# Optimization experiments

Measured on AMD Instinct MI355X. Metric: run time of the kernel, lower is better.

Reference implementation:

```python
import jax, jax.numpy as jnp
import numpy as np

DIM = 320; HEADS = 8; DHEAD = 40; CTX_DIM = 768
INNER = HEADS * DHEAD; FF_INNER = 4 * DIM
B = 1; N = 4096; M = 77
SCALE = DHEAD ** -0.5


def setup_inputs() -> dict:
    key = jax.random.key(0)
    ks = jax.random.split(key, 16)
    p = lambda i, shape: jax.random.normal(ks[i], shape, dtype=jnp.float32) * 0.02
    return {
        "x": jax.random.normal(ks[0], (B, N, DIM), dtype=jnp.float32),
        "context": jax.random.normal(ks[1], (B, M, CTX_DIM), dtype=jnp.float32),
        "focused_attention_mask": jax.random.uniform(ks[2], (1, M, M), dtype=jnp.float32),
        "g1": jnp.ones((DIM,), jnp.float32), "b1": jnp.zeros((DIM,), jnp.float32),
        "g2": jnp.ones((DIM,), jnp.float32), "b2": jnp.zeros((DIM,), jnp.float32),
        "g3": jnp.ones((DIM,), jnp.float32), "b3": jnp.zeros((DIM,), jnp.float32),
        "Wq1": p(3, (DIM, INNER)), "Wk1": p(4, (DIM, INNER)), "Wv1": p(5, (DIM, INNER)),
        "Wo1": p(6, (INNER, DIM)), "bo1": jnp.zeros((DIM,), jnp.float32),
        "Wq2": p(7, (DIM, INNER)), "Wk2": p(8, (CTX_DIM, INNER)), "Wv2": p(9, (CTX_DIM, INNER)),
        "Wo2": p(10, (INNER, DIM)), "bo2": jnp.zeros((DIM,), jnp.float32),
        "Wff1": p(11, (DIM, 2 * FF_INNER)), "bff1": jnp.zeros((2 * FF_INNER,), jnp.float32),
        "Wff2": p(12, (FF_INNER, DIM)), "bff2": jnp.zeros((DIM,), jnp.float32),
        "use_fca": 1,
    }


def _ln(x, g, b):
    mu = x.mean(-1, keepdims=True)
    var = jnp.mean((x - mu) ** 2, -1, keepdims=True)
    return (x - mu) * jax.lax.rsqrt(var + 1e-5) * g + b


def _attn(xn, ctx, Wq, Wk, Wv, Wo, bo, fam, use_fca):
    b, n, _ = xn.shape
    heads = lambda t: t.reshape(b, t.shape[1], HEADS, DHEAD).transpose(0, 2, 1, 3)  # b h n d
    q, k, v = heads(xn @ Wq), heads(ctx @ Wk), heads(ctx @ Wv)
    sim = jnp.einsum('bhid,bhjd->bhij', q, k) * SCALE
    if use_fca:
        m = fam.shape[-1]  # fam: [1, m, m], batch must be 1 (repeat_interleave semantics)
        fw = jnp.einsum('bhqk,dk->bhqd', sim[..., :m], fam[0])
        fw = jnp.minimum(jnp.abs(fw), 1.0)
        fw = fw / (jnp.max(fw, axis=-1, keepdims=True) + 1e-6)
        fw = (fw > 0.6).astype(sim.dtype)
        sim = sim.at[..., :m].add((fw - 1.0) * 50.0)
    a = jax.nn.softmax(sim, axis=-1)
    o = jnp.einsum('bhij,bhjd->bhid', a, v).transpose(0, 2, 1, 3).reshape(b, n, INNER)
    return o @ Wo + bo


def reference(x, context, focused_attention_mask,
              g1, b1, g2, b2, g3, b3,
              Wq1, Wk1, Wv1, Wo1, bo1,
              Wq2, Wk2, Wv2, Wo2, bo2,
              Wff1, bff1, Wff2, bff2, use_fca):
    # attn1: self-attention (context=None in original -> use_fca forced to 0)
    h1 = _ln(x, g1, b1)
    x = _attn(h1, h1, Wq1, Wk1, Wv1, Wo1, bo1, None, 0) + x
    # attn2: cross-attention with focused-attention mask
    h2 = _ln(x, g2, b2)
    x = _attn(h2, context, Wq2, Wk2, Wv2, Wo2, bo2, focused_attention_mask, int(use_fca)) + x
    # GEGLU feed-forward
    h3 = _ln(x, g3, b3)
    proj = h3 @ Wff1 + bff1
    a_, gate = jnp.split(proj, 2, axis=-1)
    x = (a_ * jax.nn.gelu(gate, approximate=False)) @ Wff2 + bff2 + x
    return x
```

## Files before the change

### kernel.cpp

```cpp
#include <hip/hip_runtime.h>
#include <math.h>

typedef __bf16 bf16_t;
typedef __bf16 bf16x8 __attribute__((ext_vector_type(8)));
typedef __bf16 bf16x4 __attribute__((ext_vector_type(4)));
typedef float  f32x4  __attribute__((ext_vector_type(4)));
typedef _Float16 f16_t;
typedef _Float16 f16x4 __attribute__((ext_vector_type(4)));
typedef _Float16 f16x8 __attribute__((ext_vector_type(8)));
typedef __fp16 hf16x2 __attribute__((ext_vector_type(2)));

static constexpr float ATT_SCALE = 0.15811388300841897f;
static constexpr float SC2 = 0.22811031f;
static constexpr float LOG2E = 1.4426950408889634f;

__device__ __forceinline__ bf16_t f2b(float f) {
  unsigned u = __float_as_uint(f);
  u = (u + 0x7fffu + ((u >> 16) & 1u)) >> 16;
  unsigned short s = (unsigned short)u;
  bf16_t r;
  *(unsigned short*)&r = s;
  return r;
}
__device__ __forceinline__ float b2f(bf16_t b) {
  unsigned short s = *(const unsigned short*)&b;
  return __uint_as_float(((unsigned)s) << 16);
}
__device__ __forceinline__ void sto(float v, float* p)  { *p = v; }
__device__ __forceinline__ void sto(float v, bf16_t* p) { *p = f2b(v); }
__device__ __forceinline__ unsigned pkh2(float a, float b) {
  hf16x2 h = __builtin_amdgcn_cvt_pkrtz(a, b);
  return *(unsigned*)&h;
}

__global__ __launch_bounds__(256) void prep_kernel(
    const float* __restrict__ Wq1, const float* __restrict__ Wk1, const float* __restrict__ Wv1,
    const float* __restrict__ Wo1, const float* __restrict__ Wq2,
    const float* __restrict__ Wk2, const float* __restrict__ Wv2, const float* __restrict__ Wo2,
    const float* __restrict__ Wff1, const float* __restrict__ Wff2,
    const float* __restrict__ fam,
    bf16_t* __restrict__ wqkvt, bf16_t* __restrict__ wo1t, float* __restrict__ wkv2t,
    bf16_t* __restrict__ wo2t, bf16_t* __restrict__ wff1t, bf16_t* __restrict__ wff2t,
    bf16_t* __restrict__ wq2th, bf16_t* __restrict__ wq2tl,
    bf16_t* __restrict__ famh, bf16_t* __restrict__ faml,
    bf16_t* __restrict__ zpad)
{
  const int T1 = 960*320;
  const int T2 = T1 + 320*320;
  const int T3 = T2 + 768*640;
  const int T4 = T3 + 320*320;
  const int T5 = T4 + 2560*320;
  const int T6 = T5 + 320*1280;
  const int T7 = T6 + 320*320;
  const int T8 = T7 + 96*96;
  const int T9 = T8 + 135168;
  for (int i = blockIdx.x*256 + threadIdx.x; i < T9; i += gridDim.x*256) {
    if (i < T1) {
      int n = i / 320, k = i - n*320;
      float v = (n < 320) ? Wq1[k*320+n] * SC2
              : (n < 640) ? Wk1[k*320+n-320] : Wv1[k*320+n-640];
      wqkvt[i] = f2b(v);
    } else if (i < T2) {
      int e = i - T1; int n = e / 320, k = e - n*320;
      wo1t[e] = f2b(Wo1[k*320+n]);
    } else if (i < T3) {
      int e = i - T2; int n = e / 768, k = e - n*768;
      wkv2t[e] = (n < 320) ? Wk2[k*320+n] : Wv2[k*320+n-320];
    } else if (i < T4) {
      int e = i - T3; int n = e / 320, k = e - n*320;
      wo2t[e] = f2b(Wo2[k*320+n]);
    } else if (i < T5) {
      int e = i - T4; int n = e / 320, k = e - n*320;
      wff1t[e] = f2b(Wff1[(size_t)k*2560+n]);
    } else if (i < T6) {
      int e = i - T5; int n = e / 1280, k = e - n*1280;
      wff2t[e] = f2b(Wff2[k*320+n]);
    } else if (i < T7) {
      int e = i - T6; int n = e / 320, k = e - n*320;
      float v = Wq2[k*320+n];
      bf16_t h = f2b(v);
      wq2th[e] = h;
      wq2tl[e] = f2b(v - b2f(h));
    } else if (i < T8) {
      int e = i - T7; int d = e / 96, k = e - d*96;
      float v = (d < 77 && k < 77) ? fam[d*77 + k] : 0.f;
      bf16_t h = f2b(v);
      famh[e] = h;
      faml[e] = f2b(v - b2f(h));
    } else {
      zpad[i - T8] = f2b(0.f);
    }
  }
}

template<typename OT>
__global__ __launch_bounds__(256) void ln_kernel(
    const float* __restrict__ x, const float* __restrict__ g, const float* __restrict__ b,
    OT* __restrict__ out)
{
  const int lane = threadIdx.x & 63;
  const int row = blockIdx.x * 4 + (threadIdx.x >> 6);
  const float* xr = x + (size_t)row * 320;
  float v[5], s = 0.f, s2 = 0.f;
#pragma unroll
  for (int i = 0; i < 5; i++) { v[i] = xr[lane + i*64]; s += v[i]; s2 += v[i]*v[i]; }
#pragma unroll
  for (int o = 32; o; o >>= 1) { s += __shfl_xor(s, o); s2 += __shfl_xor(s2, o); }
  float mu = s * (1.f/320.f);
  float rs = rsqrtf(fmaxf(s2*(1.f/320.f) - mu*mu, 0.f) + 1e-5f);
#pragma unroll
  for (int i = 0; i < 5; i++) {
    int c = lane + i*64;
    sto((v[i]-mu)*rs*g[c] + b[c], &out[(size_t)row*320 + c]);
  }
}

__global__ __launch_bounds__(256) void ln2_split_kernel(
    const float* __restrict__ x, const float* __restrict__ g, const float* __restrict__ b,
    bf16_t* __restrict__ hi, bf16_t* __restrict__ lo)
{
  const int lane = threadIdx.x & 63;
  const int row = blockIdx.x * 4 + (threadIdx.x >> 6);
  const float* xr = x + (size_t)row * 320;
  float v[5], s = 0.f, s2 = 0.f;
#pragma unroll
  for (int i = 0; i < 5; i++) { v[i] = xr[lane + i*64]; s += v[i]; s2 += v[i]*v[i]; }
#pragma unroll
  for (int o = 32; o; o >>= 1) { s += __shfl_xor(s, o); s2 += __shfl_xor(s2, o); }
  float mu = s * (1.f/320.f);
  float rs = rsqrtf(fmaxf(s2*(1.f/320.f) - mu*mu, 0.f) + 1e-5f);
#pragma unroll
  for (int i = 0; i < 5; i++) {
    int c = lane + i*64;
    float y = (v[i]-mu)*rs*g[c] + b[c];
    bf16_t h = f2b(y);
    hi[(size_t)row*320 + c] = h;
    lo[(size_t)row*320 + c] = f2b(y - b2f(h));
  }
}

__global__ __launch_bounds__(256) void kv2_dot_kernel(
    const float* __restrict__ ctx, const float* __restrict__ wkv2t,
    bf16_t* __restrict__ k2h, bf16_t* __restrict__ k2l, bf16_t* __restrict__ v2t)
{
  const int gid = blockIdx.x*16 + (threadIdx.x >> 4);
  const int q = threadIdx.x & 15;
  const int m = gid / 640, n = gid - m*640;
  const float4* a = (const float4*)(ctx + (size_t)m*768);
  const float4* b = (const float4*)(wkv2t + (size_t)n*768);
  float acc = 0.f;
#pragma unroll
  for (int i = 0; i < 12; i++) {
    float4 av = a[i*16+q], bv = b[i*16+q];
    acc += av.x*bv.x + av.y*bv.y + av.z*bv.z + av.w*bv.w;
  }
#pragma unroll
  for (int o = 8; o; o >>= 1) acc += __shfl_xor(acc, o);
  if (q == 0) {
    if (n < 320) {
      int h = n / 40, d = n - h*40;
      int i = h*6144 + m*64 + d;
      bf16_t hh = f2b(acc);
      k2h[i] = hh;
      k2l[i] = f2b(acc - b2f(hh));
    } else {
      int n2 = n - 320; int h = n2 / 40, d = n2 - h*40;
      v2t[h*4608 + d*96 + m] = f2b(acc);
    }
  }
}

__global__ __launch_bounds__(256) void repack_vt_kernel(
    const bf16_t* __restrict__ qkvb, f16_t* __restrict__ vpack, bf16_t* __restrict__ kpack)
{
  __shared__ f16_t T[64*44];
  const int tid = threadIdx.x;
  const int t0 = blockIdx.x * 64, h = blockIdx.y;
  for (int e = tid; e < 320; e += 256) {
    int t = e / 5, c8 = (e - t*5) * 8;
    bf16x8 v = *(const bf16x8*)(qkvb + (size_t)(t0+t)*960 + 640 + h*40 + c8);
    f16_t* dst = &T[t*44 + c8];
#pragma unroll
    for (int j = 0; j < 8; j++) dst[j] = (f16_t)b2f(v[j]);
  }
  __syncthreads();
  for (int e = tid; e < 3072; e += 256) {
    int dt = e >> 10;
    int r  = e & 1023;
    int g2 = r >> 9, o = r & 511;
    int lane = o >> 3, j = o & 7;
    int qd = lane >> 4, ln = lane & 15;
    int d = dt*16 + ln;
    int key = g2*32 + ((j & 4) ? 16 : 0) + qd*4 + (j & 3);
    float val;
    if (d < 40)       val = (float)T[key*44 + d];
    else if (d == 40) val = 1.0f;
    else              val = 0.0f;
    vpack[(((size_t)h*3 + dt)*128 + (t0 >> 5) + g2)*512 + o] = (f16_t)val;
  }
  for (int e = tid; e < 2560; e += 256) {
    int g = e / 640, o = e - g*640;
    int key = t0 + g*16;
    bf16_t val;
    if (o < 512) {
      int lane = o >> 3, j = o & 7;
      int qd = lane >> 4, ln = lane & 15;
      val = qkvb[(size_t)(key + ln)*960 + 320 + h*40 + qd*8 + j];
    } else {
      int o2 = o - 512; int ln = o2 >> 3, j = o2 & 7;
      val = qkvb[(size_t)(key + ln)*960 + 320 + h*40 + 32 + j];
    }
    kpack[((size_t)h*256 + (t0 >> 4) + g)*640 + o] = val;
  }
}

__global__ __launch_bounds__(256, 4) void flash_self_kernel(
    const bf16_t* __restrict__ qkvb, const bf16_t* __restrict__ kpack,
    const f16_t* __restrict__ vpack,
    float* __restrict__ opart, float* __restrict__ lpart)
{
  __shared__ float Red[6144];
  const int tid = threadIdx.x;
  const int w = tid >> 6, lane = tid & 63;
  const int ln = lane & 15, qd = lane >> 4;
  const int qh = w >> 1, kh = w & 1;
  const int h = blockIdx.x & 7;
  const int q0 = (blockIdx.x >> 3) * 64;
  const int split = blockIdx.y;

  const int kgbase = h*256 + kh*2;
  const int vgbase = h*384 + kh;
  const int lko = lane*8;

  bf16x8 zero8 = {};
  bf16x8 bq[2][2];
#pragma unroll
  for (int nt = 0; nt < 2; nt++) {
    const bf16_t* qp = qkvb + (size_t)(q0 + qh*32 + nt*16 + ln)*960 + h*40;
    bq[nt][0] = *(const bf16x8*)(qp + qd*8);
    bq[nt][1] = (qd == 0) ? *(const bf16x8*)(qp + 32) : zero8;
  }

  f32x4 zero4 = {0.f,0.f,0.f,0.f};
  f32x4 oacc[3][2];
#pragma unroll
  for (int a = 0; a < 3; a++)
#pragma unroll
    for (int b = 0; b < 2; b++) oacc[a][b] = zero4;

#define FS_LOADK(DST, K0)                                                       \
  {                                                                             \
    const bf16_t* kp_ = kpack + ((size_t)kgbase + ((K0) >> 4)) * 640;           \
    DST[0][0] = *(const bf16x8*)(kp_ + lko);                                    \
    DST[0][1] = (qd == 0) ? *(const bf16x8*)(kp_ + 512 + ln*8) : zero8;         \
    DST[1][0] = *(const bf16x8*)(kp_ + 640 + lko);                              \
    DST[1][1] = (qd == 0) ? *(const bf16x8*)(kp_ + 1152 + ln*8) : zero8;        \
  }

#define FS_LOADV(DST, K0)                                                       \
  {                                                                             \
    _Pragma("unroll")                                                           \
    for (int dt_ = 0; dt_ < 3; dt_++)                                           \
      DST[dt_] = *(const f16x8*)(vpack + ((size_t)vgbase + dt_*128 + ((K0) >> 5)) * 512 + lko); \
  }

#define FS_COMPUTE(KA, VA)                                                      \
  {                                                                             \
    _Pragma("unroll")                                                           \
    for (int nt = 0; nt < 2; nt++) {                                            \
      f32x4 s0 = __builtin_amdgcn_mfma_f32_16x16x32_bf16(KA[0][0], bq[nt][0], zero4, 0,0,0); \
      s0 = __builtin_amdgcn_mfma_f32_16x16x32_bf16(KA[0][1], bq[nt][1], s0, 0,0,0); \
      f32x4 s1 = __builtin_amdgcn_mfma_f32_16x16x32_bf16(KA[1][0], bq[nt][0], zero4, 0,0,0); \
      s1 = __builtin_amdgcn_mfma_f32_16x16x32_bf16(KA[1][1], bq[nt][1], s1, 0,0,0); \
      uint4 u_;                                                                 \
      u_.x = pkh2(__builtin_amdgcn_exp2f(s0[0]), __builtin_amdgcn_exp2f(s0[1])); \
      u_.y = pkh2(__builtin_amdgcn_exp2f(s0[2]), __builtin_amdgcn_exp2f(s0[3])); \
      u_.z = pkh2(__builtin_amdgcn_exp2f(s1[0]), __builtin_amdgcn_exp2f(s1[1])); \
      u_.w = pkh2(__builtin_amdgcn_exp2f(s1[2]), __builtin_amdgcn_exp2f(s1[3])); \
      f16x8 pb = *(f16x8*)&u_;                                                  \
      _Pragma("unroll")                                                         \
      for (int dt = 0; dt < 3; dt++)                                            \
        oacc[dt][nt] = __builtin_amdgcn_mfma_f32_16x16x32_f16(VA[dt], pb, oacc[dt][nt], 0,0,0); \
    }                                                                           \
  }

  bf16x8 ka[2][2], kb[2][2];
  f16x8 va[3], vb[3];
  FS_LOADK(ka, split*2048);
#pragma unroll 1
  for (int kt = 0; kt < 32; kt += 2) {
    const int k0 = split*2048 + kt*64;
    FS_LOADV(va, k0);
    FS_LOADK(kb, k0 + 64);
    FS_COMPUTE(ka, va);
    FS_LOADV(vb, k0 + 64);
    FS_LOADK(ka, (kt + 2 < 32) ? (k0 + 128) : split*2048);
    FS_COMPUTE(kb, vb);
  }
#undef FS_LOADK
#undef FS_LOADV
#undef FS_COMPUTE

#pragma unroll
  for (int nt = 0; nt < 2; nt++)
#pragma unroll
    for (int dt = 0; dt < 3; dt++)
      *(f32x4*)&Red[((w*2 + nt)*3 + dt)*256 + ln*16 + qd*4] = oacc[dt][nt];
  __syncthreads();
  float* obase = opart + ((size_t)(split*8 + h)*4096 + q0)*40;
  const int qh2 = tid >> 7, lq = (tid >> 3) & 15, dbase = tid & 7;
#pragma unroll
  for (int nt = 0; nt < 2; nt++) {
#pragma unroll
    for (int i = 0; i < 5; i++) {
      int d = dbase + i*8;
      int dt = d >> 4, dr = d & 15;
      float v = Red[(((qh2*2 + 0)*2 + nt)*3 + dt)*256 + lq*16 + dr]
              + Red[(((qh2*2 + 1)*2 + nt)*3 + dt)*256 + lq*16 + dr];
      obase[(size_t)(qh2*32 + nt*16 + lq)*40 + d] = v;
    }
    if (dbase == 0) {
      float l = Red[(((qh2*2 + 0)*2 + nt)*3 + 2)*256 + lq*16 + 8]
              + Red[(((qh2*2 + 1)*2 + nt)*3 + 2)*256 + lq*16 + 8];
      lpart[(size_t)(split*8 + h)*4096 + q0 + qh2*32 + nt*16 + lq] = l;
    }
  }
}

__global__ __launch_bounds__(256) void merge_o1_kernel(
    const float* __restrict__ op, const float* __restrict__ lp, bf16_t* __restrict__ o1a)
{
  int i = blockIdx.x*256 + threadIdx.x;
  int q = i / 320, c = i - q*320;
  int h = c / 40, d = c - h*40;
  size_t base = ((size_t)h*4096 + q)*40 + d;
  float l = lp[h*4096 + q] + lp[32768 + h*4096 + q];
  float o = op[base] + op[base + 1310720];
  o1a[i] = f2b(o / l);
}

__global__ __launch_bounds__(256) void attn_cross_kernel(
    const float* __restrict__ q2, const bf16_t* __restrict__ k2h, const bf16_t* __restrict__ k2l,
    const bf16_t* __restrict__ famh, const bf16_t* __restrict__ faml,
    const bf16_t* __restrict__ v2t, const int* __restrict__ use_fca,
    bf16_t* __restrict__ o2)
{
  __shared__ bf16_t SMh[4][16*96];
  __shared__ bf16_t SMl[4][16*96];
  __shared__ bf16_t PAs[4][16*96];
  const int tid = threadIdx.x;
  const int w = tid >> 6, lane = tid & 63;
  const int ln = lane & 15, qd = lane >> 4;
  const int h = blockIdx.x & 7;
  const int q0 = (blockIdx.x >> 3)*64 + w*16;
  const int fca = use_fca[0];
  bf16_t* smh = SMh[w];
  bf16_t* sml = SMl[w];
  bf16_t* pa  = PAs[w];

  {
    bf16x4 z = {};
    int q = lane >> 2, c = 80 + (lane & 3)*4;
    *(bf16x4*)&smh[q*96 + c] = z;
    *(bf16x4*)&sml[q*96 + c] = z;
    *(bf16x4*)&pa [q*96 + c] = z;
  }

  bf16x8 zero8 = {};
  bf16x8 aqh0, aql0, aqh1 = zero8, aql1 = zero8;
  {
    const float* qp = q2 + (size_t)(q0 + ln)*320 + h*40;
    float4 v0 = *(const float4*)(qp + qd*8);
    float4 v1 = *(const float4*)(qp + qd*8 + 4);
    float qv[8] = {v0.x,v0.y,v0.z,v0.w,v1.x,v1.y,v1.z,v1.w};
#pragma unroll
    for (int i = 0; i < 8; i++) {
      bf16_t hh = f2b(qv[i]);
      aqh0[i] = hh; aql0[i] = f2b(qv[i] - b2f(hh));
    }
    if (qd == 0) {
      float4 u0 = *(const float4*)(qp + 32);
      float4 u1 = *(const float4*)(qp + 36);
      float uv[8] = {u0.x,u0.y,u0.z,u0.w,u1.x,u1.y,u1.z,u1.w};
#pragma unroll
      for (int i = 0; i < 8; i++) {
        bf16_t hh = f2b(uv[i]);
        aqh1[i] = hh; aql1[i] = f2b(uv[i] - b2f(hh));
      }
    }
  }

  f32x4 zero4 = {0.f,0.f,0.f,0.f};
  float ss[5][4];
#pragma unroll
  for (int nt = 0; nt < 5; nt++) {
    const bf16_t* kb = k2h + ((size_t)h*96 + nt*16 + ln)*64 + qd*8;
    const bf16_t* kl = k2l + ((size_t)h*96 + nt*16 + ln)*64 + qd*8;
    bf16x8 kh0 = *(const bf16x8*)kb;
    bf16x8 kh1 = *(const bf16x8*)(kb + 32);
    bf16x8 kl0 = *(const bf16x8*)kl;
    bf16x8 kl1 = *(const bf16x8*)(kl + 32);
    f32x4 s;
    s = __builtin_amdgcn_mfma_f32_16x16x32_bf16(aqh0, kl0, zero4, 0, 0, 0);
    s = __builtin_amdgcn_mfma_f32_16x16x32_bf16(aql0, kh0, s, 0, 0, 0);
    s = __builtin_amdgcn_mfma_f32_16x16x32_bf16(aqh0, kh0, s, 0, 0, 0);
    s = __builtin_amdgcn_mfma_f32_16x16x32_bf16(aqh1, kl1, s, 0, 0, 0);
    s = __builtin_amdgcn_mfma_f32_16x16x32_bf16(aql1, kh1, s, 0, 0, 0);
    s = __builtin_amdgcn_mfma_f32_16x16x32_bf16(aqh1, kh1, s, 0, 0, 0);
#pragma unroll
    for (int r = 0; r < 4; r++) {
      float sv = s[r] * ATT_SCALE;
      ss[nt][r] = sv;
      bf16_t hh = f2b(sv);
      smh[(qd*4 + r)*96 + nt*16 + ln] = hh;
      sml[(qd*4 + r)*96 + nt*16 + ln] = f2b(sv - b2f(hh));
    }
  }

  f32x4 facc[5];
#pragma unroll
  for (int nt = 0; nt < 5; nt++) facc[nt] = zero4;
#pragma unroll
  for (int c = 0; c < 3; c++) {
    bf16x8 sah = *(const bf16x8*)&smh[ln*96 + c*32 + qd*8];
    bf16x8 sal = *(const bf16x8*)&sml[ln*96 + c*32 + qd*8];
#pragma unroll
    for (int nt = 0; nt < 5; nt++) {
      bf16x8 fh8 = *(const bf16x8*)(famh + ((size_t)(nt*16 + ln))*96 + c*32 + qd*8);
      bf16x8 fl8 = *(const bf16x8*)(faml + ((size_t)(nt*16 + ln))*96 + c*32 + qd*8);
      facc[nt] = __builtin_amdgcn_mfma_f32_16x16x32_bf16(sah, fl8, facc[nt], 0, 0, 0);
      facc[nt] = __builtin_amdgcn_mfma_f32_16x16x32_bf16(sal, fh8, facc[nt], 0, 0, 0);
      facc[nt] = __builtin_amdgcn_mfma_f32_16x16x32_bf16(sah, fh8, facc[nt], 0, 0, 0);
    }
  }

  float pr[5][4];
  if (fca) {
    float fwv[5][4], fm[4];
#pragma unroll
    for (int nt = 0; nt < 5; nt++)
#pragma unroll
      for (int r = 0; r < 4; r++) fwv[nt][r] = fminf(fabsf(facc[nt][r]), 1.f);
#pragma unroll
    for (int r = 0; r < 4; r++) {
      float m = fmaxf(fmaxf(fwv[0][r], fwv[1][r]), fmaxf(fwv[2][r], fmaxf(fwv[3][r], fwv[4][r])));
#pragma unroll
      for (int o = 8; o; o >>= 1) m = fmaxf(m, __shfl_xor(m, o));
      fm[r] = m;
    }
#pragma unroll
    for (int nt = 0; nt < 5; nt++)
#pragma unroll
      for (int r = 0; r < 4; r++) {
        float lg = ss[nt][r] - ((fwv[nt][r] > 0.6f*(fm[r] + 1e-6f)) ? 0.f : 50.f);
        pr[nt][r] = __builtin_amdgcn_exp2f(lg * LOG2E);
      }
  } else {
#pragma unroll
    for (int nt = 0; nt < 5; nt++)
#pragma unroll
      for (int r = 0; r < 4; r++)
        pr[nt][r] = __builtin_amdgcn_exp2f(ss[nt][r] * LOG2E);
  }
  if (ln >= 13) {
#pragma unroll
    for (int r = 0; r < 4; r++) pr[4][r] = 0.f;
  }
  float l_[4] = {0.f,0.f,0.f,0.f};
#pragma unroll
  for (int nt = 0; nt < 5; nt++)
#pragma unroll
    for (int r = 0; r < 4; r++) {
      l_[r] += pr[nt][r];
      pa[(qd*4 + r)*96 + nt*16 + ln] = f2b(pr[nt][r]);
    }
#pragma unroll
  for (int r = 0; r < 4; r++)
#pragma unroll
    for (int o = 8; o; o >>= 1) l_[r] += __shfl_xor(l_[r], o);

  f32x4 oacc[3];
#pragma unroll
  for (int nt = 0; nt < 3; nt++) oacc[nt] = zero4;
#pragma unroll
  for (int c = 0; c < 3; c++) {
    bf16x8 paf = *(const bf16x8*)&pa[ln*96 + c*32 + qd*8];
#pragma unroll
    for (int nt = 0; nt < 3; nt++) {
      bf16x8 vb = *(const bf16x8*)(v2t + ((size_t)h*48 + nt*16 + ln)*96 + c*32 + qd*8);
      oacc[nt] = __builtin_amdgcn_mfma_f32_16x16x32_bf16(paf, vb, oacc[nt], 0, 0, 0);
    }
  }
  float inv[4];
#pragma unroll
  for (int r = 0; r < 4; r++) inv[r] = 1.f / l_[r];
#pragma unroll
  for (int nt = 0; nt < 3; nt++) {
    int d = nt*16 + ln;
    if (d < 40) {
#pragma unroll
      for (int r = 0; r < 4; r++)
        o2[(size_t)(q0 + qd*4 + r)*320 + h*40 + d] = f2b(oacc[nt][r]*inv[r]);
    }
  }
}

template<int OUT_BF16>
__global__ __launch_bounds__(256) void gemm_bf16_kernel(
    const bf16_t* __restrict__ A, const bf16_t* __restrict__ Bt,
    const float* __restrict__ bias, const float* __restrict__ resid,
    void* __restrict__ Cout, int M, int N, int K)
{
  __shared__ bf16_t As[128][72];
  __shared__ bf16_t Bs[64][72];
  const int tid = threadIdx.x;
  const int m0 = blockIdx.x * 128, n0 = blockIdx.y * 64;
  const int w = tid >> 6, lane = tid & 63;
  const int wr = w >> 1, wc = w & 1;
  const int ln = lane & 15, qd = lane >> 4;
  f32x4 zero = {0.f, 0.f, 0.f, 0.f};
  f32x4 acc[4][2];
#pragma unroll
  for (int a = 0; a < 4; a++)
#pragma unroll
    for (int b = 0; b < 2; b++) acc[a][b] = zero;

  for (int k0 = 0; k0 < K; k0 += 64) {
    __syncthreads();
#pragma unroll
    for (int i = 0; i < 4; i++) {
      int vid = tid + i*256;
      int r = vid >> 3, c8 = (vid & 7) * 8;
      *(bf16x8*)&As[r][c8] = *(const bf16x8*)(A + (size_t)(m0+r)*K + k0 + c8);
    }
#pragma unroll
    for (int i = 0; i < 2; i++) {
      int vid = tid + i*256;
      int r = vid >> 3, c8 = (vid & 7) * 8;
      *(bf16x8*)&Bs[r][c8] = *(const bf16x8*)(Bt + (size_t)(n0+r)*K + k0 + c8);
    }
    __syncthreads();
#pragma unroll
    for (int c = 0; c < 2; c++) {
      bf16x8 af[4], bfr[2];
#pragma unroll
      for (int mt = 0; mt < 4; mt++)
        af[mt] = *(const bf16x8*)&As[wr*64 + mt*16 + ln][c*32 + qd*8];
#pragma unroll
      for (int nt = 0; nt < 2; nt++)
        bfr[nt] = *(const bf16x8*)&Bs[wc*32 + nt*16 + ln][c*32 + qd*8];
#pragma unroll
      for (int mt = 0; mt < 4; mt++)
#pragma unroll
        for (int nt = 0; nt < 2; nt++)
          acc[mt][nt] = __builtin_amdgcn_mfma_f32_16x16x32_bf16(af[mt], bfr[nt], acc[mt][nt], 0, 0, 0);
    }
  }
#pragma unroll
  for (int mt = 0; mt < 4; mt++)
#pragma unroll
    for (int nt = 0; nt < 2; nt++)
#pragma unroll
      for (int r = 0; r < 4; r++) {
        int gm = m0 + wr*64 + mt*16 + qd*4 + r;
        int gn = n0 + wc*32 + nt*16 + ln;
        float v = acc[mt][nt][r];
        if (bias)  v += bias[gn];
        if (resid) v += resid[(size_t)gm*N + gn];
        if (OUT_BF16) sto(v, &((bf16_t*)Cout)[(size_t)gm*N + gn]);
        else          sto(v, &((float*)Cout)[(size_t)gm*N + gn]);
      }
}

template<int OUT_BF16>
__global__ __launch_bounds__(256) void gemm_bf16_32_kernel(
    const bf16_t* __restrict__ A, const bf16_t* __restrict__ Bt,
    const float* __restrict__ bias, const float* __restrict__ resid,
    void* __restrict__ Cout, int M, int N, int K)
{
  __shared__ bf16_t As[32][72];
  __shared__ bf16_t Bs[64][72];
  const int tid = threadIdx.x;
  const int m0 = blockIdx.x * 32, n0 = blockIdx.y * 64;
  const int w = tid >> 6, lane = tid & 63;
  const int wr = w >> 1, wc = w & 1;
  const int ln = lane & 15, qd = lane >> 4;
  f32x4 zero = {0.f, 0.f, 0.f, 0.f};
  f32x4 acc[2];
  acc[0] = zero; acc[1] = zero;

  for (int k0 = 0; k0 < K; k0 += 64) {
    __syncthreads();
    {
      int r = tid >> 3, c8 = (tid & 7) * 8;
      *(bf16x8*)&As[r][c8] = *(const bf16x8*)(A + (size_t)(m0+r)*K + k0 + c8);
    }
#pragma unroll
    for (int i = 0; i < 2; i++) {
      int vid = tid + i*256;
      int r = vid >> 3, c8 = (vid & 7) * 8;
      *(bf16x8*)&Bs[r][c8] = *(const bf16x8*)(Bt + (size_t)(n0+r)*K + k0 + c8);
    }
    __syncthreads();
#pragma unroll
    for (int c = 0; c < 2; c++) {
      bf16x8 af = *(const bf16x8*)&As[wr*16 + ln][c*32 + qd*8];
#pragma unroll
      for (int nt = 0; nt < 2; nt++) {
        bf16x8 bfr = *(const bf16x8*)&Bs[wc*32 + nt*16 + ln][c*32 + qd*8];
        acc[nt] = __builtin_amdgcn_mfma_f32_16x16x32_bf16(af, bfr, acc[nt], 0, 0, 0);
      }
    }
  }
#pragma unroll
  for (int nt = 0; nt < 2; nt++)
#pragma unroll
    for (int r = 0; r < 4; r++) {
      int gm = m0 + wr*16 + qd*4 + r;
      int gn = n0 + wc*32 + nt*16 + ln;
      float v = acc[nt][r];
      if (bias)  v += bias[gn];
      if (resid) v += resid[(size_t)gm*N + gn];
      if (OUT_BF16) sto(v, &((bf16_t*)Cout)[(size_t)gm*N + gn]);
      else          sto(v, &((float*)Cout)[(size_t)gm*N + gn]);
    }
}

__global__ __launch_bounds__(256) void gemm3_32_kernel(
    const bf16_t* __restrict__ Ah, const bf16_t* __restrict__ Al,
    const bf16_t* __restrict__ Bth, const bf16_t* __restrict__ Btl,
    float* __restrict__ C, int M, int N, int K)
{
  __shared__ bf16_t Ash[32][72];
  __shared__ bf16_t Asl[32][72];
  __shared__ bf16_t Bsh[64][72];
  __shared__ bf16_t Bsl[64][72];
  const int tid = threadIdx.x;
  const int m0 = blockIdx.x * 32, n0 = blockIdx.y * 64;
  const int w = tid >> 6, lane = tid & 63;
  const int wr = w >> 1, wc = w & 1;
  const int ln = lane & 15, qd = lane >> 4;
  f32x4 zero = {0.f, 0.f, 0.f, 0.f};
  f32x4 acc[2];
  acc[0] = zero; acc[1] = zero;

  for (int k0 = 0; k0 < K; k0 += 64) {
    __syncthreads();
    {
      int r = tid >> 3, c8 = (tid & 7) * 8;
      *(bf16x8*)&Ash[r][c8] = *(const bf16x8*)(Ah + (size_t)(m0+r)*K + k0 + c8);
      *(bf16x8*)&Asl[r][c8] = *(const bf16x8*)(Al + (size_t)(m0+r)*K + k0 + c8);
    }
#pragma unroll
    for (int i = 0; i < 2; i++) {
      int vid = tid + i*256;
      int r = vid >> 3, c8 = (vid & 7) * 8;
      *(bf16x8*)&Bsh[r][c8] = *(const bf16x8*)(Bth + (size_t)(n0+r)*K + k0 + c8);
      *(bf16x8*)&Bsl[r][c8] = *(const bf16x8*)(Btl + (size_t)(n0+r)*K + k0 + c8);
    }
    __syncthreads();
#pragma unroll
    for (int c = 0; c < 2; c++) {
      bf16x8 afh = *(const bf16x8*)&Ash[wr*16 + ln][c*32 + qd*8];
      bf16x8 afl = *(const bf16x8*)&Asl[wr*16 + ln][c*32 + qd*8];
#pragma unroll
      for (int nt = 0; nt < 2; nt++) {
        bf16x8 bfh = *(const bf16x8*)&Bsh[wc*32 + nt*16 + ln][c*32 + qd*8];
        bf16x8 bfl = *(const bf16x8*)&Bsl[wc*32 + nt*16 + ln][c*32 + qd*8];
        acc[nt] = __builtin_amdgcn_mfma_f32_16x16x32_bf16(afh, bfl, acc[nt], 0, 0, 0);
        acc[nt] = __builtin_amdgcn_mfma_f32_16x16x32_bf16(afl, bfh, acc[nt], 0, 0, 0);
        acc[nt] = __builtin_amdgcn_mfma_f32_16x16x32_bf16(afh, bfh, acc[nt], 0, 0, 0);
      }
    }
  }
#pragma unroll
  for (int nt = 0; nt < 2; nt++)
#pragma unroll
    for (int r = 0; r < 4; r++) {
      int gm = m0 + wr*16 + qd*4 + r;
      int gn = n0 + wc*32 + nt*16 + ln;
      C[(size_t)gm*N + gn] = acc[nt][r];
    }
}

__global__ __launch_bounds__(256) void gemm_geglu_kernel(
    const bf16_t* __restrict__ A, const bf16_t* __restrict__ Bt,
    const float* __restrict__ bias, bf16_t* __restrict__ gg, int K)
{
  __shared__ bf16_t As[128][72];
  __shared__ bf16_t Ba[64][72];
  __shared__ bf16_t Bg[64][72];
  const int tid = threadIdx.x;
  const int m0 = blockIdx.x * 128, n0 = blockIdx.y * 64;
  const int w = tid >> 6, lane = tid & 63;
  const int wr = w >> 1, wc = w & 1;
  const int ln = lane & 15, qd = lane >> 4;
  f32x4 zero = {0.f, 0.f, 0.f, 0.f};
  f32x4 acca[4][2], accg[4][2];
#pragma unroll
  for (int a = 0; a < 4; a++)
#pragma unroll
    for (int b = 0; b < 2; b++) { acca[a][b] = zero; accg[a][b] = zero; }

  for (int k0 = 0; k0 < K; k0 += 64) {
    __syncthreads();
#pragma unroll
    for (int i = 0; i < 4; i++) {
      int vid = tid + i*256;
      int r = vid >> 3, c8 = (vid & 7) * 8;
      *(bf16x8*)&As[r][c8] = *(const bf16x8*)(A + (size_t)(m0+r)*K + k0 + c8);
    }
#pragma unroll
    for (int i = 0; i < 2; i++) {
      int vid = tid + i*256;
      int r = vid >> 3, c8 = (vid & 7) * 8;
      *(bf16x8*)&Ba[r][c8] = *(const bf16x8*)(Bt + (size_t)(n0+r)*K + k0 + c8);
      *(bf16x8*)&Bg[r][c8] = *(const bf16x8*)(Bt + (size_t)(n0+r+1280)*K + k0 + c8);
    }
    __syncthreads();
#pragma unroll
    for (int c = 0; c < 2; c++) {
      bf16x8 af[4], ba[2], bg[2];
#pragma unroll
      for (int mt = 0; mt < 4; mt++)
        af[mt] = *(const bf16x8*)&As[wr*64 + mt*16 + ln][c*32 + qd*8];
#pragma unroll
      for (int nt = 0; nt < 2; nt++) {
        ba[nt] = *(const bf16x8*)&Ba[wc*32 + nt*16 + ln][c*32 + qd*8];
        bg[nt] = *(const bf16x8*)&Bg[wc*32 + nt*16 + ln][c*32 + qd*8];
      }
#pragma unroll
      for (int mt = 0; mt < 4; mt++)
#pragma unroll
        for (int nt = 0; nt < 2; nt++) {
          acca[mt][nt] = __builtin_amdgcn_mfma_f32_16x16x32_bf16(af[mt], ba[nt], acca[mt][nt], 0, 0, 0);
          accg[mt][nt] = __builtin_amdgcn_mfma_f32_16x16x32_bf16(af[mt], bg[nt], accg[mt][nt], 0, 0, 0);
        }
    }
  }
#pragma unroll
  for (int mt = 0; mt < 4; mt++)
#pragma unroll
    for (int nt = 0; nt < 2; nt++)
#pragma unroll
      for (int r = 0; r < 4; r++) {
        int gm = m0 + wr*64 + mt*16 + qd*4 + r;
        int gn = n0 + wc*32 + nt*16 + ln;
        float va = acca[mt][nt][r] + bias[gn];
        float vg = accg[mt][nt][r] + bias[1280 + gn];
        float ge = 0.5f * vg * (1.f + erff(vg * 0.70710678118654752f));
        gg[(size_t)gm*1280 + gn] = f2b(va * ge);
      }
}

extern "C" void kernel_launch(void* const* d_in, const int* in_sizes, int n_in,
                              void* d_out, int out_size, void* d_ws, size_t ws_size,
                              hipStream_t stream)
{
  const float* x    = (const float*)d_in[0];
  const float* ctx  = (const float*)d_in[1];
  const float* fam  = (const float*)d_in[2];
  const float* g1   = (const float*)d_in[3];
  const float* b1   = (const float*)d_in[4];
  const float* g2   = (const float*)d_in[5];
  const float* b2   = (const float*)d_in[6];
  const float* g3   = (const float*)d_in[7];
  const float* b3   = (const float*)d_in[8];
  const float* Wq1  = (const float*)d_in[9];
  const float* Wk1  = (const float*)d_in[10];
  const float* Wv1  = (const float*)d_in[11];
  const float* Wo1  = (const float*)d_in[12];
  const float* bo1  = (const float*)d_in[13];
  const float* Wq2  = (const float*)d_in[14];
  const float* Wk2  = (const float*)d_in[15];
  const float* Wv2  = (const float*)d_in[16];
  const float* Wo2  = (const float*)d_in[17];
  const float* bo2  = (const float*)d_in[18];
  const float* Wff1 = (const float*)d_in[19];
  const float* bff1 = (const float*)d_in[20];
  const float* Wff2 = (const float*)d_in[21];
  const float* bff2 = (const float*)d_in[22];
  const int*   ufca = (const int*)d_in[23];

  char* ws = (char*)d_ws;
  bf16_t* qkvb = (bf16_t*)(ws + 0);
  f16_t*  vpack = (f16_t*)(ws + 7864320);
  bf16_t* o1a  = (bf16_t*)(ws + 11010048);
  bf16_t* kpack = (bf16_t*)(ws + 11010048);
  bf16_t* h1b  = (bf16_t*)(ws + 13631488);
  bf16_t* h2hi = (bf16_t*)(ws + 16252928);
  bf16_t* h2lo = (bf16_t*)(ws + 18874368);
  float*  x2   = (float*)(ws + 21495808);
  float*  q2   = (float*)(ws + 26738688);
  bf16_t* o2   = (bf16_t*)(ws + 32178688);
  float*  x3   = (float*)(ws + 34800128);
  bf16_t* h3b  = (bf16_t*)(ws + 40043008);
  bf16_t* wqkvt = (bf16_t*)(ws + 42664448);
  bf16_t* wo1t  = (bf16_t*)(ws + 43278848);
  float*  wkv2t = (float*)(ws + 43483648);
  bf16_t* wo2t  = (bf16_t*)(ws + 45449728);
  bf16_t* wff1t = (bf16_t*)(ws + 45654528);
  bf16_t* wff2t = (bf16_t*)(ws + 47292928);
  float*  lpart = (float*)(ws + 48112128);
  bf16_t* wq2th = (bf16_t*)(ws + 48374272);
  bf16_t* wq2tl = (bf16_t*)(ws + 48579072);
  bf16_t* famh  = (bf16_t*)(ws + 48783872);
  bf16_t* faml  = (bf16_t*)(ws + 48802304);
  bf16_t* k2h   = (bf16_t*)(ws + 48820736);
  bf16_t* k2l   = (bf16_t*)(ws + 48919040);
  bf16_t* v2t   = (bf16_t*)(ws + 49017344);
  float*  opart = (float*)(ws + 21495808);
  bf16_t* gg   = (bf16_t*)(ws + 21495808);

  float* xout = (float*)d_out;

  prep_kernel<<<2048, 256, 0, stream>>>(Wq1, Wk1, Wv1, Wo1, Wq2, Wk2, Wv2, Wo2, Wff1, Wff2, fam,
                                        wqkvt, wo1t, wkv2t, wo2t, wff1t, wff2t, wq2th, wq2tl,
                                        famh, faml, k2h);
  ln_kernel<bf16_t><<<1024, 256, 0, stream>>>(x, g1, b1, h1b);
  gemm_bf16_kernel<1><<<dim3(32,15), 256, 0, stream>>>(h1b, wqkvt, nullptr, nullptr, qkvb, 4096, 960, 320);
  repack_vt_kernel<<<dim3(64,8), 256, 0, stream>>>(qkvb, vpack, kpack);
  flash_self_kernel<<<dim3(512,2), 256, 0, stream>>>(qkvb, kpack, vpack, opart, lpart);
  merge_o1_kernel<<<5120, 256, 0, stream>>>(opart, lpart, o1a);
  gemm_bf16_32_kernel<0><<<dim3(128,5), 256, 0, stream>>>(o1a, wo1t, bo1, x, x2, 4096, 320, 320);
  ln2_split_kernel<<<1024, 256, 0, stream>>>(x2, g2, b2, h2hi, h2lo);
  gemm3_32_kernel<<<dim3(128,5), 256, 0, stream>>>(h2hi, h2lo, wq2th, wq2tl, q2, 4096, 320, 320);
  kv2_dot_kernel<<<3080, 256, 0, stream>>>(ctx, wkv2t, k2h, k2l, v2t);
  attn_cross_kernel<<<512, 256, 0, stream>>>(q2, k2h, k2l, famh, faml, v2t, ufca, o2);
  gemm_bf16_32_kernel<0><<<dim3(128,5), 256, 0, stream>>>(o2, wo2t, bo2, x2, x3, 4096, 320, 320);
  ln_kernel<bf16_t><<<1024, 256, 0, stream>>>(x3, g3, b3, h3b);
  gemm_geglu_kernel<<<dim3(32,20), 256, 0, stream>>>(h3b, wff1t, bff1, gg, 320);
  gemm_bf16_32_kernel<0><<<dim3(128,5), 256, 0, stream>>>(gg, wff2t, bff2, x3, xout, 4096, 320, 1280);
}
```

Baseline: 274.6 us.

## Replace grid-level split-K in self-attention with in-block 4-way key split and fused merge

The self-attention kernel previously split the key range across two grid blocks, wrote fp32 partial outputs and row sums to global memory, and then ran a separate merge kernel. Now each block uses 512 threads (8 waves), with 4 waves per query half covering interleaved key chunks across the full key range. The partials are reduced in shared memory and normalized, and bf16 output is written directly. This removes a kernel launch and the fp32 partial round trip, in exchange for larger blocks, twice the shared memory, and half as many blocks in the grid.

```diff
diff --git a/kernel.cpp b/kernel.cpp
--- a/kernel.cpp
+++ b/kernel.cpp
@@ -214,19 +214,18 @@
   }
 }
 
-__global__ __launch_bounds__(256, 4) void flash_self_kernel(
+__global__ __launch_bounds__(512, 4) void flash_self_kernel(
     const bf16_t* __restrict__ qkvb, const bf16_t* __restrict__ kpack,
     const f16_t* __restrict__ vpack,
-    float* __restrict__ opart, float* __restrict__ lpart)
-{
-  __shared__ float Red[6144];
+    bf16_t* __restrict__ o1a)
+{
+  __shared__ float Red[12288];
   const int tid = threadIdx.x;
   const int w = tid >> 6, lane = tid & 63;
   const int ln = lane & 15, qd = lane >> 4;
-  const int qh = w >> 1, kh = w & 1;
+  const int qh = w >> 2, kh = w & 3;
   const int h = blockIdx.x & 7;
   const int q0 = (blockIdx.x >> 3) * 64;
-  const int split = blockIdx.y;
 
   const int kgbase = h*256 + kh*2;
   const int vgbase = h*384 + kh;
@@ -286,15 +285,15 @@
 
   bf16x8 ka[2][2], kb[2][2];
   f16x8 va[3], vb[3];
-  FS_LOADK(ka, split*2048);
+  FS_LOADK(ka, 0);
 #pragma unroll 1
-  for (int kt = 0; kt < 32; kt += 2) {
-    const int k0 = split*2048 + kt*64;
+  for (int it = 0; it < 32; it += 2) {
+    const int k0 = it*128;
     FS_LOADV(va, k0);
-    FS_LOADK(kb, k0 + 64);
+    FS_LOADK(kb, k0 + 128);
     FS_COMPUTE(ka, va);
-    FS_LOADV(vb, k0 + 64);
-    FS_LOADK(ka, (kt + 2 < 32) ? (k0 + 128) : split*2048);
+    FS_LOADV(vb, k0 + 128);
+    FS_LOADK(ka, (it + 2 < 32) ? (k0 + 256) : 0);
     FS_COMPUTE(kb, vb);
   }
 #undef FS_LOADK
@@ -307,36 +306,23 @@
     for (int dt = 0; dt < 3; dt++)
       *(f32x4*)&Red[((w*2 + nt)*3 + dt)*256 + ln*16 + qd*4] = oacc[dt][nt];
   __syncthreads();
-  float* obase = opart + ((size_t)(split*8 + h)*4096 + q0)*40;
-  const int qh2 = tid >> 7, lq = (tid >> 3) & 15, dbase = tid & 7;
-#pragma unroll
-  for (int nt = 0; nt < 2; nt++) {
-#pragma unroll
-    for (int i = 0; i < 5; i++) {
-      int d = dbase + i*8;
-      int dt = d >> 4, dr = d & 15;
-      float v = Red[(((qh2*2 + 0)*2 + nt)*3 + dt)*256 + lq*16 + dr]
-              + Red[(((qh2*2 + 1)*2 + nt)*3 + dt)*256 + lq*16 + dr];
-      obase[(size_t)(qh2*32 + nt*16 + lq)*40 + d] = v;
-    }
-    if (dbase == 0) {
-      float l = Red[(((qh2*2 + 0)*2 + nt)*3 + 2)*256 + lq*16 + 8]
-              + Red[(((qh2*2 + 1)*2 + nt)*3 + 2)*256 + lq*16 + 8];
-      lpart[(size_t)(split*8 + h)*4096 + q0 + qh2*32 + nt*16 + lq] = l;
-    }
-  }
-}
-
-__global__ __launch_bounds__(256) void merge_o1_kernel(
-    const float* __restrict__ op, const float* __restrict__ lp, bf16_t* __restrict__ o1a)
-{
-  int i = blockIdx.x*256 + threadIdx.x;
-  int q = i / 320, c = i - q*320;
-  int h = c / 40, d = c - h*40;
-  size_t base = ((size_t)h*4096 + q)*40 + d;
-  float l = lp[h*4096 + q] + lp[32768 + h*4096 + q];
-  float o = op[base] + op[base + 1310720];
-  o1a[i] = f2b(o / l);
+  const int dgrp = tid & 7, lq = (tid >> 3) & 15, ntw = (tid >> 7) & 1, qh2 = tid >> 8;
+  float l = Red[(((qh2*4 + 0)*2 + ntw)*3 + 2)*256 + lq*16 + 8]
+          + Red[(((qh2*4 + 1)*2 + ntw)*3 + 2)*256 + lq*16 + 8]
+          + Red[(((qh2*4 + 2)*2 + ntw)*3 + 2)*256 + lq*16 + 8]
+          + Red[(((qh2*4 + 3)*2 + ntw)*3 + 2)*256 + lq*16 + 8];
+  float inv = 1.f / l;
+  bf16_t* obase = o1a + (size_t)(q0 + qh2*32 + ntw*16 + lq)*320 + h*40;
+#pragma unroll
+  for (int i = 0; i < 5; i++) {
+    int d = dgrp + i*8;
+    int dt = d >> 4, dr = d & 15;
+    float o = Red[(((qh2*4 + 0)*2 + ntw)*3 + dt)*256 + lq*16 + dr]
+            + Red[(((qh2*4 + 1)*2 + ntw)*3 + dt)*256 + lq*16 + dr]
+            + Red[(((qh2*4 + 2)*2 + ntw)*3 + dt)*256 + lq*16 + dr]
+            + Red[(((qh2*4 + 3)*2 + ntw)*3 + dt)*256 + lq*16 + dr];
+    obase[d] = f2b(o * inv);
+  }
 }
 
 __global__ __launch_bounds__(256) void attn_cross_kernel(
@@ -785,13 +771,13 @@
   char* ws = (char*)d_ws;
   bf16_t* qkvb = (bf16_t*)(ws + 0);
   f16_t*  vpack = (f16_t*)(ws + 7864320);
-  bf16_t* o1a  = (bf16_t*)(ws + 11010048);
   bf16_t* kpack = (bf16_t*)(ws + 11010048);
   bf16_t* h1b  = (bf16_t*)(ws + 13631488);
   bf16_t* h2hi = (bf16_t*)(ws + 16252928);
   bf16_t* h2lo = (bf16_t*)(ws + 18874368);
   float*  x2   = (float*)(ws + 21495808);
   float*  q2   = (float*)(ws + 26738688);
+  bf16_t* o1a  = (bf16_t*)(ws + 26738688);
   bf16_t* o2   = (bf16_t*)(ws + 32178688);
   float*  x3   = (float*)(ws + 34800128);
   bf16_t* h3b  = (bf16_t*)(ws + 40043008);
@@ -801,7 +787,6 @@
   bf16_t* wo2t  = (bf16_t*)(ws + 45449728);
   bf16_t* wff1t = (bf16_t*)(ws + 45654528);
   bf16_t* wff2t = (bf16_t*)(ws + 47292928);
-  float*  lpart = (float*)(ws + 48112128);
   bf16_t* wq2th = (bf16_t*)(ws + 48374272);
   bf16_t* wq2tl = (bf16_t*)(ws + 48579072);
   bf16_t* famh  = (bf16_t*)(ws + 48783872);
@@ -809,7 +794,6 @@
   bf16_t* k2h   = (bf16_t*)(ws + 48820736);
   bf16_t* k2l   = (bf16_t*)(ws + 48919040);
   bf16_t* v2t   = (bf16_t*)(ws + 49017344);
-  float*  opart = (float*)(ws + 21495808);
   bf16_t* gg   = (bf16_t*)(ws + 21495808);
 
   float* xout = (float*)d_out;
@@ -820,8 +804,7 @@
   ln_kernel<bf16_t><<<1024, 256, 0, stream>>>(x, g1, b1, h1b);
   gemm_bf16_kernel<1><<<dim3(32,15), 256, 0, stream>>>(h1b, wqkvt, nullptr, nullptr, qkvb, 4096, 960, 320);
   repack_vt_kernel<<<dim3(64,8), 256, 0, stream>>>(qkvb, vpack, kpack);
-  flash_self_kernel<<<dim3(512,2), 256, 0, stream>>>(qkvb, kpack, vpack, opart, lpart);
-  merge_o1_kernel<<<5120, 256, 0, stream>>>(opart, lpart, o1a);
+  flash_self_kernel<<<512, 512, 0, stream>>>(qkvb, kpack, vpack, o1a);
   gemm_bf16_32_kernel<0><<<dim3(128,5), 256, 0, stream>>>(o1a, wo1t, bo1, x, x2, 4096, 320, 320);
   ln2_split_kernel<<<1024, 256, 0, stream>>>(x2, g2, b2, h2hi, h2lo);
   gemm3_32_kernel<<<dim3(128,5), 256, 0, stream>>>(h2hi, h2lo, wq2th, wq2tl, q2, 4096, 320, 320);
```

Result: faster. 267.7 us (-2.5%).
